# Kernel tuning notes

Measured on AMD Instinct MI355X. Metric: run time of the kernel, lower is better.

## Reference

```python
import jax, jax.numpy as jnp
import numpy as np

N = 100000
E = 1600000
F_IN = 602
NHID = 128
N_CLS = 41


def setup_inputs() -> dict:
    key = jax.random.key(0)
    k1, k2, k3, k4 = jax.random.split(key, 4)
    x = jax.random.normal(k1, (N, F_IN), dtype=jnp.float32)
    edge_index = jax.random.randint(k2, (2, E), 0, N, dtype=jnp.int64)
    # Glorot-style scaled weights
    W1 = jax.random.normal(k3, (F_IN, NHID), dtype=jnp.float32) * (1.0 / np.sqrt(F_IN))
    b1 = jnp.zeros((NHID,), dtype=jnp.float32)
    W2 = jax.random.normal(k4, (NHID, N_CLS), dtype=jnp.float32) * (1.0 / np.sqrt(NHID))
    b2 = jnp.zeros((N_CLS,), dtype=jnp.float32)
    return {"x": x, "edge_index": edge_index, "W1": W1, "b1": b1, "W2": W2, "b2": b2}


def reference(x, edge_index, W1, b1, W2, b2):
    n = x.shape[0]
    loop = jnp.arange(n, dtype=edge_index.dtype)
    # PyG GCNConv: add self-loops, symmetric normalization D^-1/2 (A+I) D^-1/2
    src = jnp.concatenate([edge_index[0], loop])  # [E+N]
    dst = jnp.concatenate([edge_index[1], loop])  # [E+N]
    ones = jnp.ones(src.shape[0], dtype=x.dtype)
    deg = jax.ops.segment_sum(ones, dst, num_segments=n)  # in-degree incl self-loop
    dinv = jnp.where(deg > 0, jax.lax.rsqrt(deg), 0.0)
    norm = dinv[src] * dinv[dst]  # [E+N]

    def conv(h, W, b):
        h = h @ W  # transform first (smaller feature dim for gather)
        msg = h[src] * norm[:, None]  # gather + scale
        return jax.ops.segment_sum(msg, dst, num_segments=n) + b  # scatter-add

    h = jax.nn.relu(conv(x, W1, b1))
    # dropout is identity in eval mode
    out = conv(h, W2, b2)
    return jax.nn.log_softmax(out, axis=1)
```

## Files before the change

### kernel.cpp

```cpp
#include <hip/hip_runtime.h>
#include <math.h>

#define GK 602
#define GH 128
#define GC 41
#define GCP 48
#define KPAD 608
#define GS 40

typedef __bf16 bf16x8 __attribute__((ext_vector_type(8)));
typedef __bf16 bf16x4 __attribute__((ext_vector_type(4)));
typedef float f32x16 __attribute__((ext_vector_type(16)));

__device__ __forceinline__ unsigned short f2bf(float f) {
    __bf16 b = (__bf16)f;
    return __builtin_bit_cast(unsigned short, b);
}
__device__ __forceinline__ float bf2f(unsigned short u) {
    return __uint_as_float((unsigned int)u << 16);
}
__device__ __forceinline__ float bflo(unsigned int u) { return __uint_as_float(u << 16); }
__device__ __forceinline__ float bfhi(unsigned int u) { return __uint_as_float(u & 0xffff0000u); }


__global__ void k_hist(const int* __restrict__ dst, int* __restrict__ counts, int E) {
    int e = blockIdx.x * 256 + threadIdx.x;
    if (e < E) atomicAdd(&counts[dst[e]], 1);
}

__global__ void k_scan_a(const int* __restrict__ counts, int* __restrict__ row_ptr,
                         int* __restrict__ bsum, int n) {
    __shared__ int wsum[4];
    int t = threadIdx.x;
    int lane = t & 63;
    int wv = t >> 6;
    int base = blockIdx.x * 1024 + t * 4;
    int v[4];
    int s = 0;
#pragma unroll
    for (int j = 0; j < 4; ++j) {
        int idx = base + j;
        v[j] = (idx < n) ? counts[idx] : 0;
        s += v[j];
    }
    int incl = s;
#pragma unroll
    for (int o = 1; o < 64; o <<= 1) {
        int x = __shfl_up(incl, o);
        if (lane >= o) incl += x;
    }
    if (lane == 63) wsum[wv] = incl;
    __syncthreads();
    int woff = 0;
#pragma unroll
    for (int i = 0; i < 3; ++i) woff += (i < wv) ? wsum[i] : 0;
    if (t == 255) bsum[blockIdx.x] = woff + incl;
    int off = woff + incl - s;
#pragma unroll
    for (int j = 0; j < 4; ++j) {
        int idx = base + j;
        if (idx < n) row_ptr[idx] = off;
        off += v[j];
    }
}

__global__ void k_scan_b(int* __restrict__ bsum, int nb) {
    __shared__ int sh[256];
    int t = threadIdx.x;
    int v = (t < nb) ? bsum[t] : 0;
    sh[t] = v;
    __syncthreads();
    for (int o = 1; o < 256; o <<= 1) {
        int x = (t >= o) ? sh[t - o] : 0;
        __syncthreads();
        sh[t] += x;
        __syncthreads();
    }
    if (t < nb) bsum[t] = sh[t] - v;
}

__global__ void k_scan_c(int* __restrict__ row_ptr, const int* __restrict__ bsum,
                         const int* __restrict__ counts, float* __restrict__ dinv,
                         int* __restrict__ cursor, int n, int E) {
    int i = blockIdx.x * 256 + threadIdx.x;
    if (i < n) {
        int rp = row_ptr[i] + bsum[i >> 10];
        row_ptr[i] = rp;
        cursor[i] = rp;
        dinv[i] = rsqrtf((float)(counts[i] + 1));
    }
    if (i == 0) row_ptr[n] = E;
}

__global__ void k_fill(const int* __restrict__ src, const int* __restrict__ dst,
                       const float* __restrict__ dinv,
                       int* __restrict__ cursor, int2* __restrict__ meta, int E) {
    int e = blockIdx.x * 256 + threadIdx.x;
    if (e < E) {
        int s = src[e];
        int d = dst[e];
        int p = atomicAdd(&cursor[d], 1);
        float w = dinv[s] * dinv[d];
        meta[p] = make_int2(s, __float_as_int(w));
    }
}


__global__ void k_prepW1(const float* __restrict__ W1, unsigned short* __restrict__ W1T) {
    int i = blockIdx.x * 256 + threadIdx.x;
    if (i >= GH * KPAD) return;
    int n = i / KPAD;
    int k = i - n * KPAD;
    float v = (k < GK) ? W1[(size_t)k * GH + n] : 0.f;
    W1T[i] = f2bf(v);
}


struct AF { float4 v0, v1, v2, v3; };

__device__ __forceinline__ AF loadA(const float* __restrict__ xr, int kb, bool tail) {
    AF r;
    if (!tail) {
        r.v0 = *(const float4*)(xr + kb);
        r.v1 = *(const float4*)(xr + kb + 4);
        r.v2 = *(const float4*)(xr + kb + 16);
        r.v3 = *(const float4*)(xr + kb + 20);
    } else {
        float tv[8], tw[8];
#pragma unroll
        for (int j = 0; j < 8; ++j) {
            int k0_ = kb + j;
            int k1_ = kb + 16 + j;
            tv[j] = (k0_ < GK) ? xr[k0_] : 0.f;
            tw[j] = (k1_ < GK) ? xr[k1_] : 0.f;
        }
        r.v0 = make_float4(tv[0], tv[1], tv[2], tv[3]);
        r.v1 = make_float4(tv[4], tv[5], tv[6], tv[7]);
        r.v2 = make_float4(tw[0], tw[1], tw[2], tw[3]);
        r.v3 = make_float4(tw[4], tw[5], tw[6], tw[7]);
    }
    return r;
}

__device__ __forceinline__ bf16x8 cvt8(float4 a, float4 b) {
    bf16x8 r;
    r[0] = (__bf16)a.x; r[1] = (__bf16)a.y; r[2] = (__bf16)a.z; r[3] = (__bf16)a.w;
    r[4] = (__bf16)b.x; r[5] = (__bf16)b.y; r[6] = (__bf16)b.z; r[7] = (__bf16)b.w;
    return r;
}

__device__ __forceinline__ void stageB(const unsigned short* __restrict__ W1T,
                                       __bf16* __restrict__ Bsb, int tid, int k0) {
#pragma unroll
    for (int s = 0; s < 2; ++s) {
        int slot = tid + 256 * s;
        int n = slot >> 2;
        int j = slot & 3;
        uint4 v = *(const uint4*)&W1T[(size_t)n * KPAD + k0 + 8 * j];
        *(uint4*)&Bsb[n * GS + 8 * j] = v;
    }
}

__global__ __launch_bounds__(256) void k_gemm1_mfma(const float* __restrict__ X,
                                                    const unsigned short* __restrict__ W1T,
                                                    unsigned short* __restrict__ Y, int M) {
    __shared__ __bf16 Bs[2][128 * GS];
    int tid = threadIdx.x;
    int lane = tid & 63;
    int w = tid >> 6;
    int row0 = blockIdx.x * 128;
    int amr = 32 * w + (lane & 31);
    int grow_base = row0 + amr;
    int arow = (grow_base < M) ? grow_base : (M - 1);
    const float* xr = X + (size_t)arow * GK;
    int kh = (lane >> 5) * 8;
    int bn = lane & 31;

    f32x16 acc[4];
#pragma unroll
    for (int c = 0; c < 4; ++c)
#pragma unroll
        for (int i = 0; i < 16; ++i) acc[c][i] = 0.f;

    stageB(W1T, Bs[0], tid, 0);
    AF a = loadA(xr, kh, false);
    __syncthreads();

    int buf = 0;
    for (int it = 0; it < 19; ++it) {
        AF an;
        if (it < 18) {
            stageB(W1T, Bs[buf ^ 1], tid, 32 * (it + 1));
            an = loadA(xr, kh + 32 * (it + 1), it == 17);
        }
        bf16x8 af0 = cvt8(a.v0, a.v1);
        bf16x8 af1 = cvt8(a.v2, a.v3);
#pragma unroll
        for (int c = 0; c < 4; ++c) {
            bf16x8 b0 = *(const bf16x8*)&Bs[buf][(32 * c + bn) * GS + kh];
            acc[c] = __builtin_amdgcn_mfma_f32_32x32x16_bf16(af0, b0, acc[c], 0, 0, 0);
        }
#pragma unroll
        for (int c = 0; c < 4; ++c) {
            bf16x8 b1 = *(const bf16x8*)&Bs[buf][(32 * c + bn) * GS + 16 + kh];
            acc[c] = __builtin_amdgcn_mfma_f32_32x32x16_bf16(af1, b1, acc[c], 0, 0, 0);
        }
        __syncthreads();
        buf ^= 1;
        a = an;
    }
#pragma unroll
    for (int c = 0; c < 4; ++c) {
#pragma unroll
        for (int reg = 0; reg < 16; ++reg) {
            int rrow = (reg & 3) + 8 * (reg >> 2) + 4 * (lane >> 5);
            int grow = row0 + 32 * w + rrow;
            int gcol = 32 * c + (lane & 31);
            if (grow < M) Y[(size_t)grow * GH + gcol] = f2bf(acc[c][reg]);
        }
    }
}


__global__ __launch_bounds__(256) void k_agg1(const unsigned int* __restrict__ H,
                                              unsigned int* __restrict__ O,
                                              const int* __restrict__ row_ptr,
                                              const int2* __restrict__ meta,
                                              const float* __restrict__ dinv,
                                              const float* __restrict__ bias, int n) {
    int wv = threadIdx.x >> 6;
    int lane = threadIdx.x & 63;
    int d = blockIdx.x * 4 + wv;
    if (d >= n) return;
    float dd = dinv[d];
    int beg = row_ptr[d], end = row_ptr[d + 1];
    unsigned int v = H[(size_t)d * 64 + lane];
    float sw = dd * dd;
    float a0 = sw * bflo(v);
    float a1 = sw * bfhi(v);
    int e = beg;
    for (; e + 8 <= end; e += 8) {
        int2 m[8];
        unsigned int u[8];
#pragma unroll
        for (int j = 0; j < 8; ++j) m[j] = meta[e + j];
#pragma unroll
        for (int j = 0; j < 8; ++j) u[j] = H[(size_t)m[j].x * 64 + lane];
#pragma unroll
        for (int j = 0; j < 8; ++j) {
            float wj = __int_as_float(m[j].y);
            a0 = fmaf(wj, bflo(u[j]), a0);
            a1 = fmaf(wj, bfhi(u[j]), a1);
        }
    }
    if (e + 4 <= end) {
        int2 m[4];
        unsigned int u[4];
#pragma unroll
        for (int j = 0; j < 4; ++j) m[j] = meta[e + j];
#pragma unroll
        for (int j = 0; j < 4; ++j) u[j] = H[(size_t)m[j].x * 64 + lane];
#pragma unroll
        for (int j = 0; j < 4; ++j) {
            float wj = __int_as_float(m[j].y);
            a0 = fmaf(wj, bflo(u[j]), a0);
            a1 = fmaf(wj, bfhi(u[j]), a1);
        }
        e += 4;
    }
    for (; e < end; ++e) {
        int2 m = meta[e];
        unsigned int u = H[(size_t)m.x * 64 + lane];
        float wj = __int_as_float(m.y);
        a0 = fmaf(wj, bflo(u), a0);
        a1 = fmaf(wj, bfhi(u), a1);
    }
    a0 = fmaxf(a0 + bias[2 * lane], 0.f);
    a1 = fmaxf(a1 + bias[2 * lane + 1], 0.f);
    O[(size_t)d * 64 + lane] = (unsigned int)f2bf(a0) | ((unsigned int)f2bf(a1) << 16);
}


__global__ __launch_bounds__(256) void k_gemm2t(const unsigned int* __restrict__ Hb,
                                                const float* __restrict__ W2,
                                                unsigned short* __restrict__ G, int n) {
    __shared__ float ws[128][GCP];
    for (int i = threadIdx.x; i < 128 * GCP; i += 256) {
        int k = i / GCP;
        int c = i - k * GCP;
        ws[k][c] = (c < GC) ? W2[k * GC + c] : 0.f;
    }
    __syncthreads();
    int r0 = blockIdx.x * 512 + threadIdx.x;
    int r1 = r0 + 256;
    bool v0 = r0 < n, v1 = r1 < n;
    float acc0[GCP], acc1[GCP];
#pragma unroll
    for (int c = 0; c < GCP; ++c) { acc0[c] = 0.f; acc1[c] = 0.f; }
    const uint2* h0 = (const uint2*)(Hb + (size_t)(v0 ? r0 : 0) * 64);
    const uint2* h1 = (const uint2*)(Hb + (size_t)(v1 ? r1 : 0) * 64);
    for (int q = 0; q < 32; ++q) {
        uint2 ua = h0[q];
        uint2 ub = h1[q];
        float va[4] = {bflo(ua.x), bfhi(ua.x), bflo(ua.y), bfhi(ua.y)};
        float vb[4] = {bflo(ub.x), bfhi(ub.x), bflo(ub.y), bfhi(ub.y)};
#pragma unroll
        for (int j = 0; j < 4; ++j) {
            int k = 4 * q + j;
#pragma unroll
            for (int cq = 0; cq < GCP / 4; ++cq) {
                float4 wv = *(const float4*)&ws[k][4 * cq];
                acc0[4 * cq + 0] = fmaf(va[j], wv.x, acc0[4 * cq + 0]);
                acc0[4 * cq + 1] = fmaf(va[j], wv.y, acc0[4 * cq + 1]);
                acc0[4 * cq + 2] = fmaf(va[j], wv.z, acc0[4 * cq + 2]);
                acc0[4 * cq + 3] = fmaf(va[j], wv.w, acc0[4 * cq + 3]);
                acc1[4 * cq + 0] = fmaf(vb[j], wv.x, acc1[4 * cq + 0]);
                acc1[4 * cq + 1] = fmaf(vb[j], wv.y, acc1[4 * cq + 1]);
                acc1[4 * cq + 2] = fmaf(vb[j], wv.z, acc1[4 * cq + 2]);
                acc1[4 * cq + 3] = fmaf(vb[j], wv.w, acc1[4 * cq + 3]);
            }
        }
    }
    if (v0) {
#pragma unroll
        for (int c = 0; c < GCP; ++c) G[(size_t)r0 * GCP + c] = f2bf(acc0[c]);
    }
    if (v1) {
#pragma unroll
        for (int c = 0; c < GCP; ++c) G[(size_t)r1 * GCP + c] = f2bf(acc1[c]);
    }
}


__global__ __launch_bounds__(256) void k_agg2(const unsigned short* __restrict__ G,
                                              float* __restrict__ out,
                                              const int* __restrict__ row_ptr,
                                              const int2* __restrict__ meta,
                                              const float* __restrict__ dinv,
                                              const float* __restrict__ b2, int n) {
    int wv = threadIdx.x >> 6;
    int lane = threadIdx.x & 63;
    int gl = (lane < GCP) ? lane : (GCP - 1);
    int d = blockIdx.x * 4 + wv;
    if (d >= n) return;
    float dd = dinv[d];
    int beg = row_ptr[d], end = row_ptr[d + 1];
    float a = dd * dd * bf2f(G[(size_t)d * GCP + gl]);
    int e = beg;
    for (; e + 8 <= end; e += 8) {
        int2 m[8];
        unsigned short u[8];
#pragma unroll
        for (int j = 0; j < 8; ++j) m[j] = meta[e + j];
#pragma unroll
        for (int j = 0; j < 8; ++j) u[j] = G[(size_t)m[j].x * GCP + gl];
#pragma unroll
        for (int j = 0; j < 8; ++j) a = fmaf(__int_as_float(m[j].y), bf2f(u[j]), a);
    }
    if (e + 4 <= end) {
        int2 m[4];
        unsigned short u[4];
#pragma unroll
        for (int j = 0; j < 4; ++j) m[j] = meta[e + j];
#pragma unroll
        for (int j = 0; j < 4; ++j) u[j] = G[(size_t)m[j].x * GCP + gl];
#pragma unroll
        for (int j = 0; j < 4; ++j) a = fmaf(__int_as_float(m[j].y), bf2f(u[j]), a);
        e += 4;
    }
    for (; e < end; ++e) {
        int2 m = meta[e];
        a = fmaf(__int_as_float(m.y), bf2f(G[(size_t)m.x * GCP + gl]), a);
    }
    float logit = (lane < GC) ? (a + b2[lane]) : -INFINITY;
    float mx = logit;
#pragma unroll
    for (int off = 32; off; off >>= 1) mx = fmaxf(mx, __shfl_xor(mx, off));
    float ex = (lane < GC) ? __expf(logit - mx) : 0.f;
    float sm = ex;
#pragma unroll
    for (int off = 32; off; off >>= 1) sm += __shfl_xor(sm, off);
    if (lane < GC) out[(size_t)d * GC + lane] = logit - mx - __logf(sm);
}


static inline size_t alignup256(size_t x) { return (x + 255) & ~(size_t)255; }

extern "C" void kernel_launch(void* const* d_in, const int* in_sizes, int n_in,
                              void* d_out, int out_size, void* d_ws, size_t ws_size,
                              hipStream_t stream) {
    const float* x  = (const float*)d_in[0];
    const int*   ei = (const int*)d_in[1];
    const float* W1 = (const float*)d_in[2];
    const float* b1 = (const float*)d_in[3];
    const float* W2 = (const float*)d_in[4];
    const float* b2 = (const float*)d_in[5];
    float* out = (float*)d_out;

    const int n = in_sizes[0] / GK;
    const int E = in_sizes[1] / 2;
    const int* src = ei;
    const int* dst = ei + E;

    char* w = (char*)d_ws;
    char* p;
    p = w; w += alignup256((size_t)n * 4);            float* dinv  = (float*)p;
    p = w; w += alignup256((size_t)n * 4);            int* counts  = (int*)p;
    p = w; w += alignup256((size_t)n * 4);            int* cursor  = (int*)p;
    p = w; w += alignup256((size_t)(n + 1) * 4);      int* row_ptr = (int*)p;
    p = w; w += alignup256(1024 * 4);                 int* bsum    = (int*)p;
    p = w; w += alignup256((size_t)E * 8);            int2* meta   = (int2*)p;
    p = w; w += alignup256((size_t)GH * KPAD * 2);    unsigned short* W1T = (unsigned short*)p;
    p = w; w += alignup256((size_t)n * GH * 2);       unsigned short* bufA = (unsigned short*)p;
    p = w; w += alignup256((size_t)n * GH * 2);       unsigned short* bufB = (unsigned short*)p;
    p = w; w += alignup256((size_t)n * GCP * 2);      unsigned short* G    = (unsigned short*)p;

    hipMemsetAsync(counts, 0, (size_t)n * 4, stream);

    int gE = (E + 255) / 256;
    int gN = (n + 255) / 256;
    int nb = (n + 1023) / 1024;

    k_hist<<<gE, 256, 0, stream>>>(dst, counts, E);
    k_scan_a<<<nb, 256, 0, stream>>>(counts, row_ptr, bsum, n);
    k_scan_b<<<1, 256, 0, stream>>>(bsum, nb);
    k_scan_c<<<gN, 256, 0, stream>>>(row_ptr, bsum, counts, dinv, cursor, n, E);
    k_fill<<<gE, 256, 0, stream>>>(src, dst, dinv, cursor, meta, E);

    k_prepW1<<<(GH * KPAD + 255) / 256, 256, 0, stream>>>(W1, W1T);
    k_gemm1_mfma<<<(n + 127) / 128, 256, 0, stream>>>(x, W1T, bufA, n);
    k_agg1<<<(n + 3) / 4, 256, 0, stream>>>((const unsigned int*)bufA, (unsigned int*)bufB,
                                            row_ptr, meta, dinv, b1, n);
    k_gemm2t<<<(n + 511) / 512, 256, 0, stream>>>((const unsigned int*)bufB, W2, G, n);
    k_agg2<<<(n + 3) / 4, 256, 0, stream>>>(G, out, row_ptr, meta, dinv, b2, n);
}
```

Baseline: 726.7 us.

## Read W1 fragments directly from global in GEMM1, deepen A prefetch, unroll aggregation by 16

```diff
diff --git a/kernel.cpp b/kernel.cpp
--- a/kernel.cpp
+++ b/kernel.cpp
@@ -6,10 +6,9 @@
 #define GC 41
 #define GCP 48
 #define KPAD 608
-#define GS 40
+#define NKT 19
 
 typedef __bf16 bf16x8 __attribute__((ext_vector_type(8)));
-typedef __bf16 bf16x4 __attribute__((ext_vector_type(4)));
 typedef float f32x16 __attribute__((ext_vector_type(16)));
 
 __device__ __forceinline__ unsigned short f2bf(float f) {
@@ -149,28 +148,14 @@
     return r;
 }
 
-__device__ __forceinline__ void stageB(const unsigned short* __restrict__ W1T,
-                                       __bf16* __restrict__ Bsb, int tid, int k0) {
-#pragma unroll
-    for (int s = 0; s < 2; ++s) {
-        int slot = tid + 256 * s;
-        int n = slot >> 2;
-        int j = slot & 3;
-        uint4 v = *(const uint4*)&W1T[(size_t)n * KPAD + k0 + 8 * j];
-        *(uint4*)&Bsb[n * GS + 8 * j] = v;
-    }
-}
-
 __global__ __launch_bounds__(256) void k_gemm1_mfma(const float* __restrict__ X,
                                                     const unsigned short* __restrict__ W1T,
                                                     unsigned short* __restrict__ Y, int M) {
-    __shared__ __bf16 Bs[2][128 * GS];
     int tid = threadIdx.x;
     int lane = tid & 63;
     int w = tid >> 6;
-    int row0 = blockIdx.x * 128;
-    int amr = 32 * w + (lane & 31);
-    int grow_base = row0 + amr;
+    int row0 = blockIdx.x * 128 + 32 * w;
+    int grow_base = row0 + (lane & 31);
     int arow = (grow_base < M) ? grow_base : (M - 1);
     const float* xr = X + (size_t)arow * GK;
     int kh = (lane >> 5) * 8;
@@ -182,39 +167,34 @@
 #pragma unroll
         for (int i = 0; i < 16; ++i) acc[c][i] = 0.f;
 
-    stageB(W1T, Bs[0], tid, 0);
-    AF a = loadA(xr, kh, false);
-    __syncthreads();
-
-    int buf = 0;
-    for (int it = 0; it < 19; ++it) {
-        AF an;
-        if (it < 18) {
-            stageB(W1T, Bs[buf ^ 1], tid, 32 * (it + 1));
-            an = loadA(xr, kh + 32 * (it + 1), it == 17);
-        }
-        bf16x8 af0 = cvt8(a.v0, a.v1);
-        bf16x8 af1 = cvt8(a.v2, a.v3);
+    AF a0 = loadA(xr, kh, false);
+    AF a1 = loadA(xr, kh + 32, false);
+
+    for (int it = 0; it < NKT; ++it) {
+        AF a2;
+        if (it + 2 < NKT) a2 = loadA(xr, kh + 32 * (it + 2), (it + 2) == (NKT - 1));
+        bf16x8 af0 = cvt8(a0.v0, a0.v1);
+        bf16x8 af1 = cvt8(a0.v2, a0.v3);
+        const unsigned short* bbase = W1T + 32 * it + kh;
 #pragma unroll
         for (int c = 0; c < 4; ++c) {
-            bf16x8 b0 = *(const bf16x8*)&Bs[buf][(32 * c + bn) * GS + kh];
+            bf16x8 b0 = *(const bf16x8*)&bbase[(size_t)(32 * c + bn) * KPAD];
             acc[c] = __builtin_amdgcn_mfma_f32_32x32x16_bf16(af0, b0, acc[c], 0, 0, 0);
         }
 #pragma unroll
         for (int c = 0; c < 4; ++c) {
-            bf16x8 b1 = *(const bf16x8*)&Bs[buf][(32 * c + bn) * GS + 16 + kh];
+            bf16x8 b1 = *(const bf16x8*)&bbase[(size_t)(32 * c + bn) * KPAD + 16];
             acc[c] = __builtin_amdgcn_mfma_f32_32x32x16_bf16(af1, b1, acc[c], 0, 0, 0);
         }
-        __syncthreads();
-        buf ^= 1;
-        a = an;
+        a0 = a1;
+        a1 = a2;
     }
 #pragma unroll
     for (int c = 0; c < 4; ++c) {
 #pragma unroll
         for (int reg = 0; reg < 16; ++reg) {
             int rrow = (reg & 3) + 8 * (reg >> 2) + 4 * (lane >> 5);
-            int grow = row0 + 32 * w + rrow;
+            int grow = row0 + rrow;
             int gcol = 32 * c + (lane & 31);
             if (grow < M) Y[(size_t)grow * GH + gcol] = f2bf(acc[c][reg]);
         }
@@ -239,7 +219,21 @@
     float a0 = sw * bflo(v);
     float a1 = sw * bfhi(v);
     int e = beg;
-    for (; e + 8 <= end; e += 8) {
+    for (; e + 16 <= end; e += 16) {
+        int2 m[16];
+        unsigned int u[16];
+#pragma unroll
+        for (int j = 0; j < 16; ++j) m[j] = meta[e + j];
+#pragma unroll
+        for (int j = 0; j < 16; ++j) u[j] = H[(size_t)m[j].x * 64 + lane];
+#pragma unroll
+        for (int j = 0; j < 16; ++j) {
+            float wj = __int_as_float(m[j].y);
+            a0 = fmaf(wj, bflo(u[j]), a0);
+            a1 = fmaf(wj, bfhi(u[j]), a1);
+        }
+    }
+    if (e + 8 <= end) {
         int2 m[8];
         unsigned int u[8];
 #pragma unroll
@@ -252,6 +246,7 @@
             a0 = fmaf(wj, bflo(u[j]), a0);
             a1 = fmaf(wj, bfhi(u[j]), a1);
         }
+        e += 8;
     }
     if (e + 4 <= end) {
         int2 m[4];
@@ -347,7 +342,17 @@
     int beg = row_ptr[d], end = row_ptr[d + 1];
     float a = dd * dd * bf2f(G[(size_t)d * GCP + gl]);
     int e = beg;
-    for (; e + 8 <= end; e += 8) {
+    for (; e + 16 <= end; e += 16) {
+        int2 m[16];
+        unsigned short u[16];
+#pragma unroll
+        for (int j = 0; j < 16; ++j) m[j] = meta[e + j];
+#pragma unroll
+        for (int j = 0; j < 16; ++j) u[j] = G[(size_t)m[j].x * GCP + gl];
+#pragma unroll
+        for (int j = 0; j < 16; ++j) a = fmaf(__int_as_float(m[j].y), bf2f(u[j]), a);
+    }
+    if (e + 8 <= end) {
         int2 m[8];
         unsigned short u[8];
 #pragma unroll
@@ -356,6 +361,7 @@
         for (int j = 0; j < 8; ++j) u[j] = G[(size_t)m[j].x * GCP + gl];
 #pragma unroll
         for (int j = 0; j < 8; ++j) a = fmaf(__int_as_float(m[j].y), bf2f(u[j]), a);
+        e += 8;
     }
     if (e + 4 <= end) {
         int2 m[4];
```

After: 828.6 us. +14.0%, slower.
